# Optimization experiments

Hardware: AMD Instinct MI355X
Metric: run time of the kernel (lower is better)

The kernel has to match this reference:

```python
import jax, jax.numpy as jnp
import numpy as np

N = 131072  # number of attention rows (batch * queries)
M = 100     # number of 2D Gaussian basis functions (10x10 grid in original repo)
TWO_PI = 6.283185307179586


def inv2x2(A):
    """Closed-form inverse and determinant of batched 2x2 matrices."""
    a = A[..., 0, 0]; b = A[..., 0, 1]; c = A[..., 1, 0]; d = A[..., 1, 1]
    det = a * d - b * c
    row0 = jnp.stack([d, -b], axis=-1)
    row1 = jnp.stack([-c, a], axis=-1)
    inv = jnp.stack([row0, row1], axis=-2) / det[..., None, None]
    return inv, det


def setup_inputs() -> dict:
    key = jax.random.key(0)
    k1, k2, k3, k4 = jax.random.split(key, 4)
    # linear canonical parameter eta = Sigma^{-1} mu
    eta = 0.5 * jax.random.normal(k1, (N, 2), dtype=jnp.float32)
    # SPD precision P so that theta[:,2:6] = -0.5 * P (valid exp-family params)
    L = 0.3 * jax.random.normal(k2, (N, 2, 2), dtype=jnp.float32)
    P = L @ jnp.swapaxes(L, -1, -2) + 0.5 * jnp.eye(2, dtype=jnp.float32)
    theta = jnp.concatenate([eta, (-0.5 * P).reshape(N, 4)], axis=1)  # [N,6]
    # Gaussian basis functions: means in [0,1]^2, small diagonal covariances
    basis_mu = jax.random.uniform(k3, (M, 2), dtype=jnp.float32)
    var = jax.random.uniform(k4, (M, 2), dtype=jnp.float32, minval=0.01, maxval=0.05)
    basis_sigma = jax.vmap(jnp.diag)(var)  # [M,2,2]
    return {"theta": theta, "basis_mu": basis_mu, "basis_sigma": basis_sigma}


def reference(theta, basis_mu, basis_sigma):
    # Sigma = symmetrized inverse of (-2 * quadratic canonical params)
    P = -2.0 * theta[:, 2:6].reshape(-1, 2, 2)          # [N,2,2]
    Pinv, _ = inv2x2(P)
    Sigma = 0.5 * (Pinv + jnp.swapaxes(Pinv, -1, -2))   # [N,2,2]
    Mu = jnp.einsum('nij,nj->ni', Sigma, theta[:, 0:2])  # [N,2]
    # r[n,j] = integral N(t; Mu_n, Sigma_n) N(t; mu_j, S_j) dt
    #        = N(Mu_n - mu_j; 0, Sigma_n + S_j)
    C = Sigma[:, None, :, :] + basis_sigma[None, :, :, :]  # [N,M,2,2]
    diff = Mu[:, None, :] - basis_mu[None, :, :]           # [N,M,2]
    Cinv, detC = inv2x2(C)
    quad = jnp.einsum('nmi,nmij,nmj->nm', diff, Cinv, diff)
    r = jnp.exp(-0.5 * quad) / (TWO_PI * jnp.sqrt(detC))   # [N,M]
    return r
```

## Files before the change

kernel.cpp:

```cpp
#include <hip/hip_runtime.h>

#define M_BASIS 100
constexpr float INV_TWO_PI = 0.15915494309189535f;

__global__ __launch_bounds__(256) void cs_kernel(
    const float* __restrict__ theta,
    const float* __restrict__ basis_mu,
    const float* __restrict__ basis_sigma,
    float* __restrict__ out,
    int N)
{
    const int lane = threadIdx.x & 63;
    const int waves_per_block = blockDim.x >> 6;
    const int wave_id = blockIdx.x * waves_per_block + (threadIdx.x >> 6);
    const int num_waves = gridDim.x * waves_per_block;

    const int j0 = lane;
    const int j1 = lane + 64;
    const bool has_j1 = (j1 < M_BASIS);

    float2 muA = ((const float2*)basis_mu)[j0];
    float4 sgA = ((const float4*)basis_sigma)[j0];
    float2 muB = make_float2(0.f, 0.f);
    float4 sgB = make_float4(1.f, 0.f, 0.f, 1.f);
    if (has_j1) {
        muB = ((const float2*)basis_mu)[j1];
        sgB = ((const float4*)basis_sigma)[j1];
    }

    for (int n = wave_id; n < N; n += num_waves) {
        const float* th = theta + n * 6;
        float2 e  = *(const float2*)(th);
        float2 qa = *(const float2*)(th + 2);
        float2 qb = *(const float2*)(th + 4);

        float p00 = -2.0f * qa.x, p01 = -2.0f * qa.y;
        float p10 = -2.0f * qb.x, p11 = -2.0f * qb.y;
        float detP = p00 * p11 - p01 * p10;
        float inv_detP = __builtin_amdgcn_rcpf(detP);
        float S00 = p11 * inv_detP;
        float S11 = p00 * inv_detP;
        float S01 = -0.5f * (p01 + p10) * inv_detP;
        float Mu0 = S00 * e.x + S01 * e.y;
        float Mu1 = S01 * e.x + S11 * e.y;

        float* orow = out + (size_t)n * M_BASIS;

        {
            float c00 = S00 + sgA.x, c01 = S01 + sgA.y;
            float c10 = S01 + sgA.z, c11 = S11 + sgA.w;
            float d0 = Mu0 - muA.x, d1 = Mu1 - muA.y;
            float detC = c00 * c11 - c01 * c10;
            float invC = __builtin_amdgcn_rcpf(detC);
            float quad = (d0 * (c11 * d0 - c01 * d1) + d1 * (c00 * d1 - c10 * d0)) * invC;
            orow[j0] = __expf(-0.5f * quad) * INV_TWO_PI * __builtin_amdgcn_rsqf(detC);
        }
        if (has_j1) {
            float c00 = S00 + sgB.x, c01 = S01 + sgB.y;
            float c10 = S01 + sgB.z, c11 = S11 + sgB.w;
            float d0 = Mu0 - muB.x, d1 = Mu1 - muB.y;
            float detC = c00 * c11 - c01 * c10;
            float invC = __builtin_amdgcn_rcpf(detC);
            float quad = (d0 * (c11 * d0 - c01 * d1) + d1 * (c00 * d1 - c10 * d0)) * invC;
            orow[j1] = __expf(-0.5f * quad) * INV_TWO_PI * __builtin_amdgcn_rsqf(detC);
        }
    }
}

extern "C" void kernel_launch(void* const* d_in, const int* in_sizes, int n_in,
                              void* d_out, int out_size, void* d_ws, size_t ws_size,
                              hipStream_t stream) {
    const float* theta      = (const float*)d_in[0];
    const float* basis_mu   = (const float*)d_in[1];
    const float* basis_sig  = (const float*)d_in[2];
    float* out = (float*)d_out;

    int N = in_sizes[0] / 6;
    int block = 256;
    int grid = 4096;
    hipLaunchKernelGGL(cs_kernel, dim3(grid), dim3(block), 0, stream,
                       theta, basis_mu, basis_sig, out, N);
}
```

Baseline: 86.97 us.

## Remap threads to four basis functions each with float4 row stores

Each block of 256 threads is split into 10 groups of 25 threads. Each group handles one row, and each thread computes 4 consecutive basis outputs and writes them with a single float4 store. The old scheme had one wave per row, which left 28 of the 64 lanes idle on the second half. This layout replaces it with denser vector stores and full use of the 250 active lanes. The grid is also halved. Six threads per block stay idle, and the float4 stores rely on each 400-byte row starting at a 16-byte-aligned address.

```diff
diff --git a/kernel.cpp b/kernel.cpp
--- a/kernel.cpp
+++ b/kernel.cpp
@@ -10,60 +10,51 @@
     float* __restrict__ out,
     int N)
 {
-    const int lane = threadIdx.x & 63;
-    const int waves_per_block = blockDim.x >> 6;
-    const int wave_id = blockIdx.x * waves_per_block + (threadIdx.x >> 6);
-    const int num_waves = gridDim.x * waves_per_block;
+    const int tid = threadIdx.x;
+    if (tid >= 250) return;
+    const int grp = tid / 25;
+    const int k   = tid - grp * 25;
+    const int j   = 4 * k;
 
-    const int j0 = lane;
-    const int j1 = lane + 64;
-    const bool has_j1 = (j1 < M_BASIS);
-
-    float2 muA = ((const float2*)basis_mu)[j0];
-    float4 sgA = ((const float4*)basis_sigma)[j0];
-    float2 muB = make_float2(0.f, 0.f);
-    float4 sgB = make_float4(1.f, 0.f, 0.f, 1.f);
-    if (has_j1) {
-        muB = ((const float2*)basis_mu)[j1];
-        sgB = ((const float4*)basis_sigma)[j1];
+    float mu0[4], mu1[4];
+    float s00[4], s01[4], s10[4], s11[4];
+#pragma unroll
+    for (int c = 0; c < 4; ++c) {
+        float2 m = ((const float2*)basis_mu)[j + c];
+        float4 s = ((const float4*)basis_sigma)[j + c];
+        mu0[c] = m.x; mu1[c] = m.y;
+        s00[c] = s.x; s01[c] = s.y; s10[c] = s.z; s11[c] = s.w;
     }
 
-    for (int n = wave_id; n < N; n += num_waves) {
-        const float* th = theta + n * 6;
+    const int rows_per_sweep = gridDim.x * 10;
+    for (int row = blockIdx.x * 10 + grp; row < N; row += rows_per_sweep) {
+        const float* th = theta + (size_t)row * 6;
         float2 e  = *(const float2*)(th);
         float2 qa = *(const float2*)(th + 2);
         float2 qb = *(const float2*)(th + 4);
 
         float p00 = -2.0f * qa.x, p01 = -2.0f * qa.y;
         float p10 = -2.0f * qb.x, p11 = -2.0f * qb.y;
-        float detP = p00 * p11 - p01 * p10;
-        float inv_detP = __builtin_amdgcn_rcpf(detP);
+        float inv_detP = __builtin_amdgcn_rcpf(p00 * p11 - p01 * p10);
         float S00 = p11 * inv_detP;
         float S11 = p00 * inv_detP;
         float S01 = -0.5f * (p01 + p10) * inv_detP;
         float Mu0 = S00 * e.x + S01 * e.y;
         float Mu1 = S01 * e.x + S11 * e.y;
 
-        float* orow = out + (size_t)n * M_BASIS;
-
-        {
-            float c00 = S00 + sgA.x, c01 = S01 + sgA.y;
-            float c10 = S01 + sgA.z, c11 = S11 + sgA.w;
-            float d0 = Mu0 - muA.x, d1 = Mu1 - muA.y;
+        float r[4];
+#pragma unroll
+        for (int c = 0; c < 4; ++c) {
+            float c00 = S00 + s00[c], c01 = S01 + s01[c];
+            float c10 = S01 + s10[c], c11 = S11 + s11[c];
+            float d0 = Mu0 - mu0[c], d1 = Mu1 - mu1[c];
             float detC = c00 * c11 - c01 * c10;
             float invC = __builtin_amdgcn_rcpf(detC);
             float quad = (d0 * (c11 * d0 - c01 * d1) + d1 * (c00 * d1 - c10 * d0)) * invC;
-            orow[j0] = __expf(-0.5f * quad) * INV_TWO_PI * __builtin_amdgcn_rsqf(detC);
+            r[c] = __expf(-0.5f * quad) * INV_TWO_PI * __builtin_amdgcn_rsqf(detC);
         }
-        if (has_j1) {
-            float c00 = S00 + sgB.x, c01 = S01 + sgB.y;
-            float c10 = S01 + sgB.z, c11 = S11 + sgB.w;
-            float d0 = Mu0 - muB.x, d1 = Mu1 - muB.y;
-            float detC = c00 * c11 - c01 * c10;
-            float invC = __builtin_amdgcn_rcpf(detC);
-            float quad = (d0 * (c11 * d0 - c01 * d1) + d1 * (c00 * d1 - c10 * d0)) * invC;
-            orow[j1] = __expf(-0.5f * quad) * INV_TWO_PI * __builtin_amdgcn_rsqf(detC);
-        }
+        float4 rv = make_float4(r[0], r[1], r[2], r[3]);
+        ((float4*)out)[(size_t)row * 25 + k] = rv;
     }
 }
 
@@ -77,7 +68,7 @@
 
     int N = in_sizes[0] / 6;
     int block = 256;
-    int grid = 4096;
+    int grid = 2048;
     hipLaunchKernelGGL(cs_kernel, dim3(grid), dim3(block), 0, stream,
                        theta, basis_mu, basis_sig, out, N);
 }
```

New measurement: 82.23 us. -5.5%, faster.
